# Kernel optimization log

Measured on AMD Instinct MI355X. Metric: run time of the kernel, lower is better.

Reference implementation:

```python
import jax, jax.numpy as jnp
import numpy as np

N = 50000        # nodes
E = 800000       # edges (avg degree 16)
D_IN = 128
HID = 128
K = 3


def cheb_edge_weights(row, col, n):
    # PyG ChebConv sym normalization with assumed lambda_max = 2.0:
    # L_hat = (2/lambda_max) * (I - D^-1/2 A D^-1/2) - I = -D^-1/2 A D^-1/2 (zero diagonal)
    mask = (row != col).astype(jnp.float32)  # remove_self_loops
    deg = jax.ops.segment_sum(mask, row, num_segments=n)
    dinv = jnp.where(deg > 0.0, jax.lax.rsqrt(jnp.maximum(deg, 1.0)), 0.0)
    return -dinv[row] * dinv[col] * mask  # [E]


def cheb_conv(x, row, col, w_edge, W, b, n):
    # Chebyshev recursion: Tx0=x, Tx1=L_hat x, Tx_k = 2 L_hat Tx_{k-1} - Tx_{k-2}
    def prop(h):  # sparse L_hat @ h via gather + segment_sum
        return jax.ops.segment_sum(w_edge[:, None] * h[col], row, num_segments=n)

    Tx0 = x
    out = Tx0 @ W[0]
    Tx1 = prop(Tx0)
    out = out + Tx1 @ W[1]
    for k in range(2, W.shape[0]):
        Tx2 = 2.0 * prop(Tx1) - Tx0
        out = out + Tx2 @ W[k]
        Tx0, Tx1 = Tx1, Tx2
    return out + b


def setup_inputs() -> dict:
    key = jax.random.key(0)
    ks = jax.random.split(key, 8)
    x = jax.random.normal(ks[0], (N, D_IN), dtype=jnp.float32)
    ei = jax.random.randint(ks[1], (2, E), 0, N, dtype=jnp.int32)
    s = 0.05
    W1 = jax.random.normal(ks[2], (K, D_IN, HID), dtype=jnp.float32) * s
    b1 = jnp.zeros((HID,), dtype=jnp.float32)
    W2 = jax.random.normal(ks[3], (K, HID, HID), dtype=jnp.float32) * s
    b2 = jnp.zeros((HID,), dtype=jnp.float32)
    W3 = jax.random.normal(ks[4], (K, HID, HID), dtype=jnp.float32) * s
    b3 = jnp.zeros((HID,), dtype=jnp.float32)
    return {"x": x, "ei": ei, "W1": W1, "b1": b1, "W2": W2, "b2": b2, "W3": W3, "b3": b3}


def reference(x, ei, W1, b1, W2, b2, W3, b3):
    row, col = ei[0], ei[1]
    w_edge = cheb_edge_weights(row, col, N)
    # layer chain: ChebConv -> ReLU -> dropout (eval mode: identity)
    h = jax.nn.relu(cheb_conv(x, row, col, w_edge, W1, b1, N))
    h = jax.nn.relu(cheb_conv(h, row, col, w_edge, W2, b2, N))
    h = jax.nn.relu(cheb_conv(h, row, col, w_edge, W3, b3, N))
    return h
```

## Files before the change

kernel.cpp:

```cpp
#include <hip/hip_runtime.h>
#include <hip/hip_bf16.h>

#define DFEAT 128

typedef _Float16 h2 __attribute__((ext_vector_type(2)));
typedef _Float16 f16x8 __attribute__((ext_vector_type(8)));
typedef float f32x4  __attribute__((ext_vector_type(4)));
typedef unsigned short u16x8 __attribute__((ext_vector_type(8)));

__device__ __forceinline__ unsigned short f16b(float f) {
    _Float16 hf = (_Float16)f;
    unsigned short b; __builtin_memcpy(&b, &hf, 2);
    return b;
}
__device__ __forceinline__ unsigned pack_f16(float lo, float hi) {
    return (unsigned)f16b(lo) | ((unsigned)f16b(hi) << 16);
}
__device__ __forceinline__ float h2f(h2 v) { float f; __builtin_memcpy(&f, &v, 4); return f; }
__device__ __forceinline__ h2 f2h(float f) { h2 v; __builtin_memcpy(&v, &f, 4); return v; }


__global__ void conv_kernel(const float2* __restrict__ x, unsigned* __restrict__ xb, int npk,
                            const float* __restrict__ W1, const float* __restrict__ W2,
                            const float* __restrict__ W3, unsigned short* __restrict__ Wt,
                            int* __restrict__ deg8, int N) {
    int id = blockIdx.x * blockDim.x + threadIdx.x;
    int gstride = gridDim.x * blockDim.x;
    for (int i = id; i < 8 * N; i += gstride) deg8[i] = 0;
    if (id < npk) {
        float2 v = x[id];
        xb[id] = pack_f16(v.x, v.y);
        return;
    }
    int id2 = id - npk;
    const int PER = 3 * DFEAT * DFEAT;
    if (id2 < 3 * PER) {
        int layer = id2 / PER;
        int rem = id2 - layer * PER;
        const float* W = (layer == 0) ? W1 : ((layer == 1) ? W2 : W3);
        int seg = rem >> 14;
        int k   = (rem >> 7) & 127;
        int nn  = rem & 127;
        float w = W[rem];
        if (seg == 0) w -= W[rem + 2 * DFEAT * DFEAT];
        else if (seg == 2) w *= 2.f;
        Wt[layer * PER + (seg << 14) + (nn << 7) + k] = f16b(w);
    }
}

__global__ void deg_kernel(const int* __restrict__ ei, int* __restrict__ deg8, int E, int N) {
    int e = blockIdx.x * blockDim.x + threadIdx.x;
    if (e < E) {
        int r = ei[e];
        int c = ei[E + e];
        if (r != c) atomicAdd(&deg8[(blockIdx.x & 7) * N + r], 1);
    }
}

__global__ __launch_bounds__(1024) void scan1_kernel(const int* __restrict__ deg8,
                                                     int* __restrict__ poff,
                                                     int* __restrict__ row_ptr,
                                                     int* __restrict__ bsum,
                                                     float* __restrict__ dinv, int n) {
    __shared__ int wsums[16];
    int t = threadIdx.x;
    int idx = blockIdx.x * 1024 + t;
    int tot = 0;
    if (idx < n) {
        int run = 0;
        #pragma unroll
        for (int p = 0; p < 8; ++p) {
            int d = deg8[p * n + idx];
            poff[p * n + idx] = run;
            run += d;
        }
        tot = run;
        dinv[idx] = (tot > 0) ? rsqrtf((float)tot) : 0.f;
    }
    int vi = tot;
    #pragma unroll
    for (int off = 1; off < 64; off <<= 1) {
        int x = __shfl_up(vi, off);
        if ((t & 63) >= off) vi += x;
    }
    if ((t & 63) == 63) wsums[t >> 6] = vi;
    __syncthreads();
    if (t < 16) {
        int s = wsums[t];
        int si = s;
        #pragma unroll
        for (int off = 1; off < 16; off <<= 1) {
            int x = __shfl_up(si, off);
            if (t >= off) si += x;
        }
        wsums[t] = si - s;
        if (t == 15) bsum[blockIdx.x] = si;
    }
    __syncthreads();
    if (idx < n) row_ptr[idx + 1] = wsums[t >> 6] + vi;
}

__global__ __launch_bounds__(1024) void scan3_kernel(int* __restrict__ row_ptr,
                                                     const int* __restrict__ bsum, int n) {
    __shared__ int soff;
    int t = threadIdx.x;
    if (t < 64) {
        int v = 0;
        for (int k = t; k < (int)blockIdx.x; k += 64) v += bsum[k];
        #pragma unroll
        for (int off = 32; off > 0; off >>= 1) v += __shfl_down(v, off);
        if (t == 0) soff = v;
    }
    __syncthreads();
    int idx = blockIdx.x * 1024 + t;
    if (idx == 0) row_ptr[0] = 0;
    if (idx < n) row_ptr[idx + 1] += soff;
}

__global__ void fill_kernel(const int* __restrict__ ei, const int* __restrict__ row_ptr,
                            int* __restrict__ poff, const float* __restrict__ dinv,
                            unsigned* __restrict__ e_cw, int E, int N) {
    int e = blockIdx.x * blockDim.x + threadIdx.x;
    if (e < E) {
        int r = ei[e];
        int c = ei[E + e];
        if (r != c) {
            int p = blockIdx.x & 7;
            int k = atomicAdd(&poff[p * N + r], 1);
            int pos = row_ptr[r] + k;
            float w = -dinv[r] * dinv[c];
            e_cw[pos] = (unsigned)c | ((unsigned)f16b(w) << 16);
        }
    }
}

__global__ __launch_bounds__(256) void prop_f16_kernel(
    const uint4* __restrict__ hin4, uint4* __restrict__ hout4,
    const int* __restrict__ row_ptr, const unsigned* __restrict__ e_cw, int n)
{
    int wv = __builtin_amdgcn_readfirstlane(threadIdx.x >> 6);
    int node = blockIdx.x * 4 + wv;
    if (node >= n) return;
    const int lane = threadIdx.x & 63;
    const int e2 = lane >> 4;
    const int s = lane & 15;
    int rs = row_ptr[node];
    int re = row_ptr[node + 1];

    h2 a0 = {(_Float16)0.f, (_Float16)0.f};
    h2 a1 = {(_Float16)0.f, (_Float16)0.f};
    h2 a2 = {(_Float16)0.f, (_Float16)0.f};
    h2 a3 = {(_Float16)0.f, (_Float16)0.f};

    for (int j = rs; j < re; j += 24) {
        uint4 vv[6]; unsigned ww[6];
        #pragma unroll
        for (int u = 0; u < 6; ++u) {
            int i0 = j + 4 * u;
            unsigned c0 = (i0     < re) ? e_cw[i0]     : 0u;
            unsigned c1 = (i0 + 1 < re) ? e_cw[i0 + 1] : 0u;
            unsigned c2 = (i0 + 2 < re) ? e_cw[i0 + 2] : 0u;
            unsigned c3 = (i0 + 3 < re) ? e_cw[i0 + 3] : 0u;
            unsigned cw = (e2 == 0) ? c0 : (e2 == 1) ? c1 : (e2 == 2) ? c2 : c3;
            ww[u] = (cw & 0xffff0000u) | (cw >> 16);
            vv[u] = hin4[(size_t)(cw & 0xffffu) * 16 + s];
        }
        #pragma unroll
        for (int u = 0; u < 6; ++u) {
            h2 wp = f2h(__uint_as_float(ww[u]));
            a0 = f2h(__uint_as_float(vv[u].x)) * wp + a0;
            a1 = f2h(__uint_as_float(vv[u].y)) * wp + a1;
            a2 = f2h(__uint_as_float(vv[u].z)) * wp + a2;
            a3 = f2h(__uint_as_float(vv[u].w)) * wp + a3;
        }
    }
    #pragma unroll
    for (int off = 16; off < 64; off <<= 1) {
        a0 = a0 + f2h(__shfl_xor(h2f(a0), off));
        a1 = a1 + f2h(__shfl_xor(h2f(a1), off));
        a2 = a2 + f2h(__shfl_xor(h2f(a2), off));
        a3 = a3 + f2h(__shfl_xor(h2f(a3), off));
    }

    if (e2 == 0) {
        uint4 o;
        o.x = __float_as_uint(h2f(a0));
        o.y = __float_as_uint(h2f(a1));
        o.z = __float_as_uint(h2f(a2));
        o.w = __float_as_uint(h2f(a3));
        hout4[(size_t)node * 16 + s] = o;
    }
}

#define WPAD 136
__global__ __launch_bounds__(256) void gemm3_mfma_kernel(
    const unsigned short* __restrict__ X0, const unsigned short* __restrict__ X1,
    const unsigned short* __restrict__ X2,
    const unsigned short* __restrict__ Wt, const float* __restrict__ bias,
    void* __restrict__ out, int n, int out_f16)
{
    __shared__ unsigned short Ws[DFEAT * WPAD];
    const int t    = threadIdx.x;
    const int wave = t >> 6;
    const int lane = t & 63;
    const int quad = lane >> 4;
    const int l16  = lane & 15;

    const int row_base = blockIdx.x * 128 + wave * 32;
    int r0 = row_base + l16;       if (r0 >= n) r0 = n - 1;
    int r1 = row_base + 16 + l16;  if (r1 >= n) r1 = n - 1;

    const unsigned short* Xps[3] = {X0, X1, X2};

    f32x4 acc[2][8];
    #pragma unroll
    for (int tt = 0; tt < 2; ++tt)
        #pragma unroll
        for (int c = 0; c < 8; ++c) acc[tt][c] = (f32x4){0.f, 0.f, 0.f, 0.f};

    const int srow = t >> 1;
    const int shalf = (t & 1) * 64;

    #pragma unroll
    for (int seg = 0; seg < 3; ++seg) {
        __syncthreads();
        const unsigned short* Wp = Wt + (seg << 14);
        #pragma unroll
        for (int i = 0; i < 8; ++i) {
            *(u16x8*)&Ws[srow * WPAD + shalf + i * 8] =
                *(const u16x8*)&Wp[srow * DFEAT + shalf + i * 8];
        }
        __syncthreads();
        const unsigned short* A0 = Xps[seg] + (size_t)r0 * DFEAT;
        const unsigned short* A1 = Xps[seg] + (size_t)r1 * DFEAT;
        #pragma unroll
        for (int kk = 0; kk < 4; ++kk) {
            const int ko = kk * 32 + quad * 8;
            f16x8 a0 = *(const f16x8*)(A0 + ko);
            f16x8 a1 = *(const f16x8*)(A1 + ko);
            #pragma unroll
            for (int c = 0; c < 8; ++c) {
                f16x8 b = *(const f16x8*)&Ws[(c * 16 + l16) * WPAD + ko];
                acc[0][c] = __builtin_amdgcn_mfma_f32_16x16x32_f16(a0, b, acc[0][c], 0, 0, 0);
                acc[1][c] = __builtin_amdgcn_mfma_f32_16x16x32_f16(a1, b, acc[1][c], 0, 0, 0);
            }
        }
    }

    #pragma unroll
    for (int tt = 0; tt < 2; ++tt) {
        int orow0 = blockIdx.x * 128 + wave * 32 + tt * 16 + quad * 4;
        #pragma unroll
        for (int c = 0; c < 8; ++c) {
            int col = c * 16 + l16;
            float bv = bias[col];
            #pragma unroll
            for (int r = 0; r < 4; ++r) {
                int orow = orow0 + r;
                if (orow < n) {
                    float v = fmaxf(acc[tt][c][r] + bv, 0.f);
                    if (out_f16)
                        ((unsigned short*)out)[(size_t)orow * DFEAT + col] = f16b(v);
                    else
                        ((float*)out)[(size_t)orow * DFEAT + col] = v;
                }
            }
        }
    }
}

extern "C" void kernel_launch(void* const* d_in, const int* in_sizes, int n_in,
                              void* d_out, int out_size, void* d_ws, size_t ws_size,
                              hipStream_t stream) {
    const float* x  = (const float*)d_in[0];
    const int*   ei = (const int*)d_in[1];
    const float* W1 = (const float*)d_in[2];
    const float* b1 = (const float*)d_in[3];
    const float* W2 = (const float*)d_in[4];
    const float* b2 = (const float*)d_in[5];
    const float* W3 = (const float*)d_in[6];
    const float* b3 = (const float*)d_in[7];

    const int N = in_sizes[0] / DFEAT;
    const int E = in_sizes[1] / 2;
    const int NPK = N * (DFEAT / 2);
    const int NB = (N + 1023) / 1024;

    unsigned* xb  = (unsigned*)d_ws;
    unsigned* t1b = xb  + NPK;
    unsigned* t2b = t1b + NPK;
    unsigned* ab  = t2b + NPK;
    unsigned short* wt = (unsigned short*)(ab + NPK);
    int*   deg8    = (int*)(wt + 3 * 3 * DFEAT * DFEAT);
    int*   poff    = deg8 + 8 * N;
    int*   row_ptr = poff + 8 * N;
    float* dinv    = (float*)(row_ptr + (N + 2));
    unsigned* e_cw = (unsigned*)(dinv + N);
    int*   bsum    = (int*)(e_cw + E);

    const int WELEM = 3 * DFEAT * DFEAT;
    const int CONVT = NPK + 3 * WELEM;
    conv_kernel<<<(CONVT + 255) / 256, 256, 0, stream>>>(
        (const float2*)x, xb, NPK, W1, W2, W3, wt, deg8, N);
    deg_kernel<<<(E + 255) / 256, 256, 0, stream>>>(ei, deg8, E, N);
    scan1_kernel<<<NB, 1024, 0, stream>>>(deg8, poff, row_ptr, bsum, dinv, N);
    scan3_kernel<<<NB, 1024, 0, stream>>>(row_ptr, bsum, N);
    fill_kernel<<<(E + 255) / 256, 256, 0, stream>>>(ei, row_ptr, poff, dinv, e_cw, E, N);

    const float* bl[3] = {b1, b2, b3};
    const unsigned* hin = xb;
    const int prop_grid = (N + 3) / 4;
    const int gemm_grid = (N + 127) / 128;
    for (int l = 0; l < 3; ++l) {
        prop_f16_kernel<<<prop_grid, 256, 0, stream>>>(
            (const uint4*)hin, (uint4*)t1b, row_ptr, e_cw, N);
        prop_f16_kernel<<<prop_grid, 256, 0, stream>>>(
            (const uint4*)t1b, (uint4*)t2b, row_ptr, e_cw, N);
        void* hout = (l == 2) ? d_out : (void*)ab;
        gemm3_mfma_kernel<<<gemm_grid, 256, 0, stream>>>(
            (const unsigned short*)hin, (const unsigned short*)t1b, (const unsigned short*)t2b,
            wt + l * WELEM, bl[l], hout, N, (l == 2) ? 0 : 1);
        hin = ab;
    }
}
```

Measured before the change: 389.2 us.

## Store fp16 features in 16-column slices so each prop block gathers one slice

Feature matrices are stored as eight 16-column slabs laid out node-major within each slab. Each prop block now handles one slab for four nodes, with 32 edges per wave in parallel, each lane loading 16 bytes. The gather working set per kernel instance shrinks so it fits in cache better. The cost is 8x more blocks, edge lists re-read per slab, and a longer shuffle reduction. The conversion, prop and GEMM read/write paths are all updated to the sliced layout.

```diff
diff --git a/kernel.cpp b/kernel.cpp
--- a/kernel.cpp
+++ b/kernel.cpp
@@ -29,7 +29,9 @@
     for (int i = id; i < 8 * N; i += gstride) deg8[i] = 0;
     if (id < npk) {
         float2 v = x[id];
-        xb[id] = pack_f16(v.x, v.y);
+        int node = id >> 6;
+        int p    = id & 63;
+        xb[((size_t)(p >> 3) * N + node) * 8 + (p & 7)] = pack_f16(v.x, v.y);
         return;
     }
     int id2 = id - npk;
@@ -139,56 +141,44 @@
     const int* __restrict__ row_ptr, const unsigned* __restrict__ e_cw, int n)
 {
     int wv = __builtin_amdgcn_readfirstlane(threadIdx.x >> 6);
-    int node = blockIdx.x * 4 + wv;
+    const int sl = blockIdx.x & 7;
+    int node = (blockIdx.x >> 3) * 4 + wv;
     if (node >= n) return;
     const int lane = threadIdx.x & 63;
-    const int e2 = lane >> 4;
-    const int s = lane & 15;
+    const int e5 = lane >> 1;
+    const int s  = lane & 1;
     int rs = row_ptr[node];
     int re = row_ptr[node + 1];
-
-    h2 a0 = {(_Float16)0.f, (_Float16)0.f};
-    h2 a1 = {(_Float16)0.f, (_Float16)0.f};
-    h2 a2 = {(_Float16)0.f, (_Float16)0.f};
-    h2 a3 = {(_Float16)0.f, (_Float16)0.f};
-
-    for (int j = rs; j < re; j += 24) {
-        uint4 vv[6]; unsigned ww[6];
-        #pragma unroll
-        for (int u = 0; u < 6; ++u) {
-            int i0 = j + 4 * u;
-            unsigned c0 = (i0     < re) ? e_cw[i0]     : 0u;
-            unsigned c1 = (i0 + 1 < re) ? e_cw[i0 + 1] : 0u;
-            unsigned c2 = (i0 + 2 < re) ? e_cw[i0 + 2] : 0u;
-            unsigned c3 = (i0 + 3 < re) ? e_cw[i0 + 3] : 0u;
-            unsigned cw = (e2 == 0) ? c0 : (e2 == 1) ? c1 : (e2 == 2) ? c2 : c3;
-            ww[u] = (cw & 0xffff0000u) | (cw >> 16);
-            vv[u] = hin4[(size_t)(cw & 0xffffu) * 16 + s];
-        }
-        #pragma unroll
-        for (int u = 0; u < 6; ++u) {
-            h2 wp = f2h(__uint_as_float(ww[u]));
-            a0 = f2h(__uint_as_float(vv[u].x)) * wp + a0;
-            a1 = f2h(__uint_as_float(vv[u].y)) * wp + a1;
-            a2 = f2h(__uint_as_float(vv[u].z)) * wp + a2;
-            a3 = f2h(__uint_as_float(vv[u].w)) * wp + a3;
-        }
-    }
-    #pragma unroll
-    for (int off = 16; off < 64; off <<= 1) {
+    const uint4* __restrict__ hsl = hin4 + (size_t)sl * n * 2;
+
+    h2 a0 = (h2){(_Float16)0.f, (_Float16)0.f};
+    h2 a1 = a0, a2 = a0, a3 = a0;
+
+    for (int j = rs; j < re; j += 32) {
+        int i0 = j + e5;
+        unsigned cw = (i0 < re) ? e_cw[i0] : 0u;
+        h2 wp = f2h(__uint_as_float((cw & 0xffff0000u) | (cw >> 16)));
+        uint4 v = hsl[(size_t)(cw & 0xffffu) * 2 + s];
+        a0 = f2h(__uint_as_float(v.x)) * wp + a0;
+        a1 = f2h(__uint_as_float(v.y)) * wp + a1;
+        a2 = f2h(__uint_as_float(v.z)) * wp + a2;
+        a3 = f2h(__uint_as_float(v.w)) * wp + a3;
+    }
+    #pragma unroll
+    for (int off = 2; off < 64; off <<= 1) {
         a0 = a0 + f2h(__shfl_xor(h2f(a0), off));
         a1 = a1 + f2h(__shfl_xor(h2f(a1), off));
         a2 = a2 + f2h(__shfl_xor(h2f(a2), off));
         a3 = a3 + f2h(__shfl_xor(h2f(a3), off));
     }
 
-    if (e2 == 0) {
+    if (lane < 2) {
         uint4 o;
         o.x = __float_as_uint(h2f(a0));
         o.y = __float_as_uint(h2f(a1));
         o.z = __float_as_uint(h2f(a2));
         o.w = __float_as_uint(h2f(a3));
-        hout4[(size_t)node * 16 + s] = o;
+        hout4[((size_t)sl * n + node) * 2 + s] = o;
     }
 }
 
@@ -231,13 +221,13 @@
                 *(const u16x8*)&Wp[srow * DFEAT + shalf + i * 8];
         }
         __syncthreads();
-        const unsigned short* A0 = Xps[seg] + (size_t)r0 * DFEAT;
-        const unsigned short* A1 = Xps[seg] + (size_t)r1 * DFEAT;
+        const unsigned short* Ab = Xps[seg];
         #pragma unroll
         for (int kk = 0; kk < 4; ++kk) {
             const int ko = kk * 32 + quad * 8;
-            f16x8 a0 = *(const f16x8*)(A0 + ko);
-            f16x8 a1 = *(const f16x8*)(A1 + ko);
+            const size_t sb = (size_t)(ko >> 4) * n * 16 + (ko & 15);
+            f16x8 a0 = *(const f16x8*)(Ab + sb + (size_t)r0 * 16);
+            f16x8 a1 = *(const f16x8*)(Ab + sb + (size_t)r1 * 16);
             #pragma unroll
             for (int c = 0; c < 8; ++c) {
                 f16x8 b = *(const f16x8*)&Ws[(c * 16 + l16) * WPAD + ko];
@@ -259,10 +249,11 @@
                 int orow = orow0 + r;
                 if (orow < n) {
                     float v = fmaxf(acc[tt][c][r] + bv, 0.f);
-                    if (out_f16)
-                        ((unsigned short*)out)[(size_t)orow * DFEAT + col] = f16b(v);
-                    else
+                    if (out_f16) {
+                        ((unsigned short*)out)[((size_t)c * n + orow) * 16 + l16] = f16b(v);
+                    } else {
                         ((float*)out)[(size_t)orow * DFEAT + col] = v;
+                    }
                 }
             }
         }
@@ -309,7 +300,7 @@
 
     const float* bl[3] = {b1, b2, b3};
     const unsigned* hin = xb;
-    const int prop_grid = (N + 3) / 4;
+    const int prop_grid = ((N + 3) / 4) * 8;
     const int gemm_grid = (N + 127) / 128;
     for (int l = 0; l < 3; ++l) {
         prop_f16_kernel<<<prop_grid, 256, 0, stream>>>(
```

Result: slower. 734.0 us (+88.6%).

## Fuse graph preprocessing kernels into one cooperative persistent kernel

Applied to the files above, without the earlier changes.

Replaces the five separate preprocessing launches (conversion and zeroing, degree count, two scan passes, CSR fill) with a single cooperative kernel. The phases are separated by grid-wide syncs, and each phase uses grid-stride loops over a grid sized from an occupancy query. The scan is rewritten as a per-wave scan followed by a single-wave carry pass over chunk sums. The aim is to remove per-launch gaps and tail effects. In exchange it adds grid.sync costs, a serial single-wave carry loop, and possibly lower parallelism in the atomic-heavy phases.

```diff
diff --git a/kernel.cpp b/kernel.cpp
--- a/kernel.cpp
+++ b/kernel.cpp
@@ -1,5 +1,8 @@
 #include <hip/hip_runtime.h>
 #include <hip/hip_bf16.h>
+#include <hip/hip_cooperative_groups.h>
+
+namespace cg = cooperative_groups;
 
 #define DFEAT 128
 
@@ -20,23 +23,32 @@
 __device__ __forceinline__ h2 f2h(float f) { h2 v; __builtin_memcpy(&v, &f, 4); return v; }
 
 
-__global__ void conv_kernel(const float2* __restrict__ x, unsigned* __restrict__ xb, int npk,
-                            const float* __restrict__ W1, const float* __restrict__ W2,
-                            const float* __restrict__ W3, unsigned short* __restrict__ Wt,
-                            int* __restrict__ deg8, int N) {
-    int id = blockIdx.x * blockDim.x + threadIdx.x;
-    int gstride = gridDim.x * blockDim.x;
-    for (int i = id; i < 8 * N; i += gstride) deg8[i] = 0;
-    if (id < npk) {
-        float2 v = x[id];
-        xb[id] = pack_f16(v.x, v.y);
-        return;
-    }
-    int id2 = id - npk;
+__global__ __launch_bounds__(256, 8) void prep_mega_kernel(
+    const float2* __restrict__ x2, const int* __restrict__ ei,
+    const float* __restrict__ W1, const float* __restrict__ W2,
+    const float* __restrict__ W3,
+    unsigned* __restrict__ xb, unsigned short* __restrict__ wt,
+    int* __restrict__ deg8, int* __restrict__ poff,
+    int* __restrict__ row_ptr, float* __restrict__ dinv,
+    unsigned* __restrict__ e_cw, int* __restrict__ csum,
+    int N, int E)
+{
+    cg::grid_group grid = cg::this_grid();
+    const int t = threadIdx.x;
+    const int tid = blockIdx.x * 256 + t;
+    const int nthreads = gridDim.x * 256;
+    const int lane = t & 63;
+
+    const int NPK = N * (DFEAT / 2);
+    for (int i = tid; i < 8 * N; i += nthreads) deg8[i] = 0;
+    for (int i = tid; i < NPK; i += nthreads) {
+        float2 v = x2[i];
+        xb[i] = pack_f16(v.x, v.y);
+    }
     const int PER = 3 * DFEAT * DFEAT;
-    if (id2 < 3 * PER) {
-        int layer = id2 / PER;
-        int rem = id2 - layer * PER;
+    for (int i = tid; i < 3 * PER; i += nthreads) {
+        int layer = i / PER;
+        int rem = i - layer * PER;
         const float* W = (layer == 0) ? W1 : ((layer == 1) ? W2 : W3);
         int seg = rem >> 14;
         int k   = (rem >> 7) & 127;
@@ -44,88 +56,72 @@
         float w = W[rem];
         if (seg == 0) w -= W[rem + 2 * DFEAT * DFEAT];
         else if (seg == 2) w *= 2.f;
-        Wt[layer * PER + (seg << 14) + (nn << 7) + k] = f16b(w);
-    }
-}
-
-__global__ void deg_kernel(const int* __restrict__ ei, int* __restrict__ deg8, int E, int N) {
-    int e = blockIdx.x * blockDim.x + threadIdx.x;
-    if (e < E) {
+        wt[layer * PER + (seg << 14) + (nn << 7) + k] = f16b(w);
+    }
+    grid.sync();
+
+    for (int e = tid; e < E; e += nthreads) {
         int r = ei[e];
         int c = ei[E + e];
-        if (r != c) atomicAdd(&deg8[(blockIdx.x & 7) * N + r], 1);
-    }
-}
-
-__global__ __launch_bounds__(1024) void scan1_kernel(const int* __restrict__ deg8,
-                                                     int* __restrict__ poff,
-                                                     int* __restrict__ row_ptr,
-                                                     int* __restrict__ bsum,
-                                                     float* __restrict__ dinv, int n) {
-    __shared__ int wsums[16];
-    int t = threadIdx.x;
-    int idx = blockIdx.x * 1024 + t;
-    int tot = 0;
-    if (idx < n) {
-        int run = 0;
-        #pragma unroll
-        for (int p = 0; p < 8; ++p) {
-            int d = deg8[p * n + idx];
-            poff[p * n + idx] = run;
-            run += d;
-        }
-        tot = run;
-        dinv[idx] = (tot > 0) ? rsqrtf((float)tot) : 0.f;
-    }
-    int vi = tot;
-    #pragma unroll
-    for (int off = 1; off < 64; off <<= 1) {
-        int x = __shfl_up(vi, off);
-        if ((t & 63) >= off) vi += x;
-    }
-    if ((t & 63) == 63) wsums[t >> 6] = vi;
-    __syncthreads();
-    if (t < 16) {
-        int s = wsums[t];
-        int si = s;
-        #pragma unroll
-        for (int off = 1; off < 16; off <<= 1) {
-            int x = __shfl_up(si, off);
-            if (t >= off) si += x;
-        }
-        wsums[t] = si - s;
-        if (t == 15) bsum[blockIdx.x] = si;
-    }
-    __syncthreads();
-    if (idx < n) row_ptr[idx + 1] = wsums[t >> 6] + vi;
-}
-
-__global__ __launch_bounds__(1024) void scan3_kernel(int* __restrict__ row_ptr,
-                                                     const int* __restrict__ bsum, int n) {
-    __shared__ int soff;
-    int t = threadIdx.x;
-    if (t < 64) {
-        int v = 0;
-        for (int k = t; k < (int)blockIdx.x; k += 64) v += bsum[k];
-        #pragma unroll
-        for (int off = 32; off > 0; off >>= 1) v += __shfl_down(v, off);
-        if (t == 0) soff = v;
-    }
-    __syncthreads();
-    int idx = blockIdx.x * 1024 + t;
-    if (idx == 0) row_ptr[0] = 0;
-    if (idx < n) row_ptr[idx + 1] += soff;
-}
-
-__global__ void fill_kernel(const int* __restrict__ ei, const int* __restrict__ row_ptr,
-                            int* __restrict__ poff, const float* __restrict__ dinv,
-                            unsigned* __restrict__ e_cw, int E, int N) {
-    int e = blockIdx.x * blockDim.x + threadIdx.x;
-    if (e < E) {
+        if (r != c) atomicAdd(&deg8[((e >> 8) & 7) * N + r], 1);
+    }
+    grid.sync();
+
+    const int NCH = (N + 63) / 64;
+    const int gwave = tid >> 6;
+    const int ngwave = nthreads >> 6;
+    for (int w = gwave; w < NCH; w += ngwave) {
+        int node = w * 64 + lane;
+        int tot = 0;
+        if (node < N) {
+            int run = 0;
+            #pragma unroll
+            for (int p = 0; p < 8; ++p) {
+                int d = deg8[p * N + node];
+                poff[p * N + node] = run;
+                run += d;
+            }
+            tot = run;
+            dinv[node] = (tot > 0) ? rsqrtf((float)tot) : 0.f;
+        }
+        int vi = tot;
+        #pragma unroll
+        for (int off = 1; off < 64; off <<= 1) {
+            int xx = __shfl_up(vi, off);
+            if (lane >= off) vi += xx;
+        }
+        if (node < N) row_ptr[node + 1] = vi;
+        if (lane == 63) csum[w] = vi;
+    }
+    grid.sync();
+
+    if (blockIdx.x == 0 && t < 64) {
+        int carry = 0;
+        for (int base = 0; base < NCH; base += 64) {
+            int v = (base + t < NCH) ? csum[base + t] : 0;
+            int vi = v;
+            #pragma unroll
+            for (int off = 1; off < 64; off <<= 1) {
+                int xx = __shfl_up(vi, off);
+                if (t >= off) vi += xx;
+            }
+            if (base + t < NCH) csum[base + t] = carry + vi - v;
+            carry += __shfl(vi, 63);
+        }
+    }
+    grid.sync();
+
+    for (int i = tid; i < N; i += nthreads) {
+        if (i == 0) row_ptr[0] = 0;
+        row_ptr[i + 1] += csum[i >> 6];
+    }
+    grid.sync();
+
+    for (int e = tid; e < E; e += nthreads) {
         int r = ei[e];
         int c = ei[E + e];
         if (r != c) {
-            int p = blockIdx.x & 7;
+            int p = (e >> 8) & 7;
             int k = atomicAdd(&poff[p * N + r], 1);
             int pos = row_ptr[r] + k;
             float w = -dinv[r] * dinv[c];
@@ -281,10 +277,9 @@
     const float* W3 = (const float*)d_in[6];
     const float* b3 = (const float*)d_in[7];
 
-    const int N = in_sizes[0] / DFEAT;
-    const int E = in_sizes[1] / 2;
+    int N = in_sizes[0] / DFEAT;
+    int E = in_sizes[1] / 2;
     const int NPK = N * (DFEAT / 2);
-    const int NB = (N + 1023) / 1024;
 
     unsigned* xb  = (unsigned*)d_ws;
     unsigned* t1b = xb  + NPK;
@@ -296,18 +291,31 @@
     int*   row_ptr = poff + 8 * N;
     float* dinv    = (float*)(row_ptr + (N + 2));
     unsigned* e_cw = (unsigned*)(dinv + N);
-    int*   bsum    = (int*)(e_cw + E);
-
+    int*   csum    = (int*)(e_cw + E);
+
+    const float2* x2 = (const float2*)x;
+
+    static int prep_blocks = 0;
+    if (prep_blocks == 0) {
+        int nb = 0;
+        hipOccupancyMaxActiveBlocksPerMultiprocessor(&nb, (const void*)prep_mega_kernel, 256, 0);
+        if (nb < 1) nb = 1;
+        long g = (long)nb * 256;
+        prep_blocks = (int)((g > 2048) ? 2048 : g);
+    }
+
+    void* args[] = {
+        (void*)&x2, (void*)&ei,
+        (void*)&W1, (void*)&W2, (void*)&W3,
+        (void*)&xb, (void*)&wt, (void*)&deg8, (void*)&poff,
+        (void*)&row_ptr, (void*)&dinv, (void*)&e_cw, (void*)&csum,
+        (void*)&N, (void*)&E
+    };
+    hipLaunchCooperativeKernel((const void*)prep_mega_kernel,
+                               dim3(prep_blocks), dim3(256), args, 0, stream);
+
+    const float* bl[3] = {b1, b2, b3};
     const int WELEM = 3 * DFEAT * DFEAT;
-    const int CONVT = NPK + 3 * WELEM;
-    conv_kernel<<<(CONVT + 255) / 256, 256, 0, stream>>>(
-        (const float2*)x, xb, NPK, W1, W2, W3, wt, deg8, N);
-    deg_kernel<<<(E + 255) / 256, 256, 0, stream>>>(ei, deg8, E, N);
-    scan1_kernel<<<NB, 1024, 0, stream>>>(deg8, poff, row_ptr, bsum, dinv, N);
-    scan3_kernel<<<NB, 1024, 0, stream>>>(row_ptr, bsum, N);
-    fill_kernel<<<(E + 255) / 256, 256, 0, stream>>>(ei, row_ptr, poff, dinv, e_cw, E, N);
-
-    const float* bl[3] = {b1, b2, b3};
     const unsigned* hin = xb;
     const int prop_grid = (N + 3) / 4;
     const int gemm_grid = (N + 127) / 128;
```

New measurement: 1.022 ms. 163% more time.
